# Kernel optimization log

Hardware: AMD Instinct MI355X
Metric: run time of the kernel (lower is better)

The kernel has to match this reference:

```python
import jax, jax.numpy as jnp
import numpy as np

T, B, I, H = 1024, 128, 512, 512
KEEP_PROB = 0.7  # dropout = 0.3


def setup_inputs() -> dict:
    key = jax.random.key(0)
    ks = jax.random.split(key, 8)
    xs = jax.random.normal(ks[0], (T, B, I), dtype=jnp.float32)
    s_in = 1.0 / np.sqrt(I)
    s_h = 1.0 / np.sqrt(H)
    W_ih1 = jax.random.normal(ks[1], (4 * H, I), dtype=jnp.float32) * s_in
    W_hh1 = jax.random.normal(ks[2], (4 * H, H), dtype=jnp.float32) * s_h
    W_ih2 = jax.random.normal(ks[3], (4 * H, H), dtype=jnp.float32) * s_h
    W_hh2 = jax.random.normal(ks[4], (4 * H, H), dtype=jnp.float32) * s_h
    b_ih1 = jnp.zeros((4 * H,), jnp.float32)
    b_hh1 = jnp.zeros((4 * H,), jnp.float32)
    b_ih2 = jnp.zeros((4 * H,), jnp.float32)
    b_hh2 = jnp.zeros((4 * H,), jnp.float32)
    # recurrent dropout mask: same Bernoulli(keep_prob) 0/1 mask for the whole sequence
    mask = jax.random.bernoulli(ks[5], KEEP_PROB, (B, H)).astype(jnp.float32)
    return {"xs": xs, "W_ih1": W_ih1, "W_hh1": W_hh1, "b_ih1": b_ih1, "b_hh1": b_hh1,
            "W_ih2": W_ih2, "W_hh2": W_hh2, "b_ih2": b_ih2, "b_hh2": b_hh2, "mask": mask}


def _lstm_cell(x, h, c, W_ih, W_hh, b_ih, b_hh):
    # PyTorch nn.LSTMCell: gates ordered (i, f, g, o)
    gates = x @ W_ih.T + b_ih + h @ W_hh.T + b_hh  # [B, 4H]
    i, f, g, o = jnp.split(gates, 4, axis=-1)
    c_new = jax.nn.sigmoid(f) * c + jax.nn.sigmoid(i) * jnp.tanh(g)
    h_new = jax.nn.sigmoid(o) * jnp.tanh(c_new)
    return h_new, c_new


def reference(xs, W_ih1, W_hh1, b_ih1, b_hh1, W_ih2, W_hh2, b_ih2, b_hh2, mask):
    drop = mask * (1.0 / KEEP_PROB)  # [B, H]; applied to both h and c (training mode)

    def step(carry, x):
        h1, c1, h2, c2 = carry
        h1, c1 = _lstm_cell(x, h1, c1, W_ih1, W_hh1, b_ih1, b_hh1)
        h1, c1 = h1 * drop, c1 * drop
        h2, c2 = _lstm_cell(h1, h2, c2, W_ih2, W_hh2, b_ih2, b_hh2)
        h2, c2 = h2 * drop, c2 * drop
        return (h1, c1, h2, c2), h2

    z = jnp.zeros((xs.shape[1], W_hh1.shape[1]), xs.dtype)
    init = (z, z, z, z)
    _, hs = jax.lax.scan(step, init, xs)
    return hs  # [T, B, H]
```

## Files before the change

kernel.cpp:

```cpp
#include <hip/hip_runtime.h>
#include <stdint.h>
#include <stddef.h>

typedef unsigned short ushort_t;
typedef __attribute__((ext_vector_type(8))) short short8;
typedef __attribute__((ext_vector_type(4))) float floatx4;

#define T_STEPS 1024
#define BATCH   128
#define HID     512
#define NBLK    128
#define NTHR    512
#define INV_KEEP 1.4285714285714286f

__device__ unsigned g_sync[4096];

struct Params {
  const float* xs;
  const float* Wih1; const float* Whh1; const float* bih1; const float* bhh1;
  const float* Wih2; const float* Whh2; const float* bih2; const float* bhh2;
  const float* mask;
  float* out;
  char* ws;
};

__device__ __forceinline__ void waitgen(unsigned target) {
  if (threadIdx.x < 64) {
    const int l = threadIdx.x;
    for (;;) {
      unsigned a = __hip_atomic_load(&g_sync[l * 32], __ATOMIC_RELAXED,
                                     __HIP_MEMORY_SCOPE_AGENT);
      unsigned b = __hip_atomic_load(&g_sync[(l + 64) * 32], __ATOMIC_RELAXED,
                                     __HIP_MEMORY_SCOPE_AGENT);
      if (__all(a >= target && b >= target)) break;
      __builtin_amdgcn_s_sleep(1);
    }
    __threadfence();
  }
  __syncthreads();
}

__device__ __forceinline__ void postgen(unsigned value) {
  __syncthreads();
  if (threadIdx.x == 0) {
    __threadfence();
    __hip_atomic_store(&g_sync[blockIdx.x * 32], value, __ATOMIC_RELAXED,
                       __HIP_MEMORY_SCOPE_AGENT);
  }
}

__device__ __forceinline__ ushort_t f2b(float a) {
  unsigned u = __float_as_uint(a);
  u += 0x7FFFu + ((u >> 16) & 1u);
  return (ushort_t)(u >> 16);
}

__global__ __launch_bounds__(NTHR, 1) void lstm_persist(Params p) {
  extern __shared__ ushort_t Wl[];

  char* ws = p.ws;
  auto H1HI = [&](int par) { return (ushort_t*)(ws + 524288 + par * 262144); };
  auto H1LO = [&](int par) { return (ushort_t*)(ws + 524288 + par * 262144 + 131072); };
  auto H2HI = [&](int par) { return (ushort_t*)(ws + 1048576 + par * 262144); };
  auto H2LO = [&](int par) { return (ushort_t*)(ws + 1048576 + par * 262144 + 131072); };
  auto XSHI = [&](int par) { return (ushort_t*)(ws + 1572864 + par * 262144); };
  auto XSLO = [&](int par) { return (ushort_t*)(ws + 1572864 + par * 262144 + 131072); };

  const int bid = blockIdx.x, tid = threadIdx.x;
  const int gtid = bid * NTHR + tid;
  const int layer = bid >> 6;
  const int c8 = bid & 63;
  const int lane = tid & 63, w = tid >> 6;
  const int jj = lane & 15, quad = lane >> 4;
  const int rbase = w * 16;

  const float* Wih = layer ? p.Wih2 : p.Wih1;
  const float* Whh = layer ? p.Whh2 : p.Whh1;
  const float* bih = layer ? p.bih2 : p.bih1;
  const float* bhh = layer ? p.bhh2 : p.bhh1;

  for (int i = tid; i < 32768; i += NTHR) {
    int e = i & 7, jjw = (i >> 3) & 15, ntw = (i >> 7) & 1, kg = i >> 8;
    int k = kg * 8 + e;
    int col = ((jjw >> 2) << 9) + c8 * 8 + ntw * 4 + (jjw & 3);
    float wv = (k < 512) ? Wih[col * 512 + k] : Whh[col * 512 + (k - 512)];
    unsigned uw = __float_as_uint(wv);
    Wl[i] = (ushort_t)(uw >> 16);
    float wf = __uint_as_float(uw & 0xFFFF0000u);
    Wl[32768 + i] = f2b(wv - wf);
  }
  {
    uint4 zz = {0u, 0u, 0u, 0u};
    uint4* dst = (uint4*)(ws + 524288);
    for (int i = gtid; i < 65536; i += NBLK * NTHR) dst[i] = zz;
  }
  {
    float v = p.xs[gtid];
    unsigned uv = __float_as_uint(v);
    XSHI(0)[gtid] = (ushort_t)(uv >> 16);
    float hf = __uint_as_float(uv & 0xFFFF0000u);
    XSLO(0)[gtid] = f2b(v - hf);
  }
  float bsum[2];
#pragma unroll
  for (int nt = 0; nt < 2; ++nt) {
    int colW = ((jj >> 2) << 9) + c8 * 8 + nt * 4 + (jj & 3);
    bsum[nt] = bih[colW] + bhh[colW];
  }
  float dpre[2][4];
  float creg[2][4];
#pragma unroll
  for (int nt = 0; nt < 2; ++nt)
#pragma unroll
    for (int e = 0; e < 4; ++e) {
      int r = rbase + quad * 4 + e;
      int hgc = c8 * 8 + nt * 4 + (lane & 3);
      dpre[nt][e] = p.mask[r * 512 + hgc] * INV_KEEP;
      creg[nt][e] = 0.f;
    }

  postgen(1);

  const int rowbyte = ((rbase + jj) * 512 + quad * 8) * 2;
  const bool dostore = (jj < 4);

#pragma unroll 1
  for (unsigned u = 0; u <= T_STEPS; ++u) {
    const bool havex = (u + 2 <= T_STEPS);
    float xv = 0.f;
    if (havex) xv = p.xs[(size_t)(u + 1) * 65536 + gtid];

    waitgen(u + 1);

    if (havex) {
      unsigned uv = __float_as_uint(xv);
      int pn = (u + 1) & 1;
      XSHI(pn)[gtid] = (ushort_t)(uv >> 16);
      float hf = __uint_as_float(uv & 0xFFFF0000u);
      XSLO(pn)[gtid] = f2b(xv - hf);
    }

    const bool active = layer ? (u >= 1) : (u < T_STEPS);
    if (active) {
      const int t = layer ? (int)u - 1 : (int)u;
      const int pu = (int)u & 1, pv = pu ^ 1;
      const ushort_t *aLoHi, *aLoLo, *aHiHi, *aHiLo;
      ushort_t *whHi, *whLo;
      if (layer == 0) {
        aLoHi = XSHI(pu); aLoLo = XSLO(pu);
        aHiHi = H1HI(pv); aHiLo = H1LO(pv);
        whHi = H1HI(pu);  whLo = H1LO(pu);
      } else {
        aLoHi = H1HI(pv); aLoLo = H1LO(pv);
        aHiHi = H2HI(pu); aHiLo = H2LO(pu);
        whHi = H2HI(pv);  whLo = H2LO(pv);
      }

      floatx4 acc[2];
      acc[0] = (floatx4){bsum[0], bsum[0], bsum[0], bsum[0]};
      acc[1] = (floatx4){bsum[1], bsum[1], bsum[1], bsum[1]};

      auto ldchunk = [&](int c, uint4* dst) {
        const char* bh = (const char*)((c < 8) ? aLoHi : aHiHi);
        const char* bl = (const char*)((c < 8) ? aLoLo : aHiLo);
        int kb = (c & 7) * 128;
#pragma unroll
        for (int ks = 0; ks < 2; ++ks) {
          int off = rowbyte + kb + ks * 64;
          dst[ks * 2 + 0] = *(const uint4*)(bh + off);
          dst[ks * 2 + 1] = *(const uint4*)(bl + off);
        }
      };

      uint4 ring[4][4];
      ldchunk(0, ring[0]);
      ldchunk(1, ring[1]);
      ldchunk(2, ring[2]);
#pragma unroll
      for (int c = 0; c < 16; ++c) {
        if (c < 13) ldchunk(c + 3, ring[(c + 3) & 3]);
        uint4* cur = ring[c & 3];
#pragma unroll
        for (int ks = 0; ks < 2; ++ks) {
          short8 ahf = *(const short8*)&cur[ks * 2 + 0];
          short8 alf = *(const short8*)&cur[ks * 2 + 1];
#pragma unroll
          for (int nt = 0; nt < 2; ++nt) {
            int o = (((c * 8 + ks * 4 + quad) * 2 + nt) * 16 + jj) * 8;
            short8 bhf = *(const short8*)&Wl[o];
            short8 blf = *(const short8*)&Wl[32768 + o];
            acc[nt] = __builtin_amdgcn_mfma_f32_16x16x32_bf16(ahf, bhf, acc[nt], 0, 0, 0);
            acc[nt] = __builtin_amdgcn_mfma_f32_16x16x32_bf16(ahf, blf, acc[nt], 0, 0, 0);
            acc[nt] = __builtin_amdgcn_mfma_f32_16x16x32_bf16(alf, bhf, acc[nt], 0, 0, 0);
          }
        }
      }

      const int sb = (lane & 48) | (lane & 3);
#pragma unroll
      for (int nt = 0; nt < 2; ++nt)
#pragma unroll
        for (int e = 0; e < 4; ++e) {
          float v = acc[nt][e];
          float gi = __shfl(v, sb + 0, 64);
          float gf = __shfl(v, sb + 4, 64);
          float gg = __shfl(v, sb + 8, 64);
          float go = __shfl(v, sb + 12, 64);
          float si = 1.f / (1.f + __expf(-gi));
          float sf = 1.f / (1.f + __expf(-gf));
          float so = 1.f / (1.f + __expf(-go));
          float tg = 2.f / (1.f + __expf(-2.f * gg)) - 1.f;
          int r = rbase + quad * 4 + e;
          int hgc = c8 * 8 + nt * 4 + (lane & 3);
          int ci = r * 512 + hgc;
          float cn = sf * creg[nt][e] + si * tg;
          float tc = 2.f / (1.f + __expf(-2.f * cn)) - 1.f;
          float hn = so * tc;
          float d = dpre[nt][e];
          hn *= d; cn *= d;
          creg[nt][e] = cn;
          if (dostore) {
            unsigned uh = __float_as_uint(hn);
            whHi[ci] = (ushort_t)(uh >> 16);
            float hf = __uint_as_float(uh & 0xFFFF0000u);
            whLo[ci] = f2b(hn - hf);
            if (layer) p.out[(size_t)t * 65536 + ci] = hn;
          }
        }
    }
    if (u < T_STEPS) postgen(u + 2);
  }
}

extern "C" void kernel_launch(void* const* d_in, const int* in_sizes, int n_in,
                              void* d_out, int out_size, void* d_ws, size_t ws_size,
                              hipStream_t stream) {
  (void)in_sizes; (void)n_in; (void)out_size; (void)ws_size;
  Params p;
  p.xs   = (const float*)d_in[0];
  p.Wih1 = (const float*)d_in[1];
  p.Whh1 = (const float*)d_in[2];
  p.bih1 = (const float*)d_in[3];
  p.bhh1 = (const float*)d_in[4];
  p.Wih2 = (const float*)d_in[5];
  p.Whh2 = (const float*)d_in[6];
  p.bih2 = (const float*)d_in[7];
  p.bhh2 = (const float*)d_in[8];
  p.mask = (const float*)d_in[9];
  p.out  = (float*)d_out;
  p.ws   = (char*)d_ws;

  static bool attr_done = false;
  if (!attr_done) {
    (void)hipFuncSetAttribute(reinterpret_cast<const void*>(lstm_persist),
                              hipFuncAttributeMaxDynamicSharedMemorySize, 131072);
    attr_done = true;
  }

  void* sym = nullptr;
  hipGetSymbolAddress(&sym, HIP_SYMBOL(g_sync));
  hipMemsetAsync(sym, 0, 4096 * sizeof(unsigned), stream);

  void* args[] = { &p };
  hipLaunchCooperativeKernel(reinterpret_cast<void*>(lstm_persist),
                             dim3(NBLK), dim3(NTHR), args, 131072, stream);
}
```

Measured before the change: 28.52 ms.

## Double block count and split K across warps with LDS reduction

Grid grows from 128 to 256 blocks, so each block covers half the batch rows. The 8 warps split the K dimension in two halves (input part and recurrent part), and the partial sums are combined through an LDS reduction buffer before the gate math. All 8 chunk loads are issued up front with inline-asm global loads and staggered vmcnt waits. The goal is more CUs working per timestep and shorter per-step latency, at the cost of an extra __syncthreads, more LDS, and twice as many blocks in the grid barrier.

```diff
diff --git a/kernel.cpp b/kernel.cpp
--- a/kernel.cpp
+++ b/kernel.cpp
@@ -5,15 +5,16 @@
 typedef unsigned short ushort_t;
 typedef __attribute__((ext_vector_type(8))) short short8;
 typedef __attribute__((ext_vector_type(4))) float floatx4;
+typedef __attribute__((ext_vector_type(4))) unsigned uintx4;
 
 #define T_STEPS 1024
 #define BATCH   128
 #define HID     512
-#define NBLK    128
+#define NBLK    256
 #define NTHR    512
 #define INV_KEEP 1.4285714285714286f
 
-__device__ unsigned g_sync[4096];
+__device__ unsigned g_sync[8192];
 
 struct Params {
   const float* xs;
@@ -32,7 +33,11 @@
                                      __HIP_MEMORY_SCOPE_AGENT);
       unsigned b = __hip_atomic_load(&g_sync[(l + 64) * 32], __ATOMIC_RELAXED,
                                      __HIP_MEMORY_SCOPE_AGENT);
-      if (__all(a >= target && b >= target)) break;
+      unsigned c = __hip_atomic_load(&g_sync[(l + 128) * 32], __ATOMIC_RELAXED,
+                                     __HIP_MEMORY_SCOPE_AGENT);
+      unsigned d = __hip_atomic_load(&g_sync[(l + 192) * 32], __ATOMIC_RELAXED,
+                                     __HIP_MEMORY_SCOPE_AGENT);
+      if (__all(a >= target && b >= target && c >= target && d >= target)) break;
       __builtin_amdgcn_s_sleep(1);
     }
     __threadfence();
@@ -55,7 +60,7 @@
   return (ushort_t)(u >> 16);
 }
 
-__global__ __launch_bounds__(NTHR, 1) void lstm_persist(Params p) {
+__global__ __launch_bounds__(NTHR, 2) void lstm_persist(Params p) {
   extern __shared__ ushort_t Wl[];
 
   char* ws = p.ws;
@@ -68,11 +73,13 @@
 
   const int bid = blockIdx.x, tid = threadIdx.x;
   const int gtid = bid * NTHR + tid;
-  const int layer = bid >> 6;
-  const int c8 = bid & 63;
+  const int layer = bid >> 7;
+  const int c8 = (bid & 127) >> 1;
+  const int bhalf = bid & 1;
   const int lane = tid & 63, w = tid >> 6;
+  const int kh = w >> 2, rg = w & 3;
   const int jj = lane & 15, quad = lane >> 4;
-  const int rbase = w * 16;
+  const int rbase = bhalf * 64 + rg * 16;
 
   const float* Wih = layer ? p.Wih2 : p.Wih1;
   const float* Whh = layer ? p.Whh2 : p.Whh1;
@@ -94,7 +101,7 @@
     uint4* dst = (uint4*)(ws + 524288);
     for (int i = gtid; i < 65536; i += NBLK * NTHR) dst[i] = zz;
   }
-  {
+  if (gtid < 65536) {
     float v = p.xs[gtid];
     unsigned uv = __float_as_uint(v);
     XSHI(0)[gtid] = (ushort_t)(uv >> 16);
@@ -122,11 +129,11 @@
   postgen(1);
 
   const int rowbyte = ((rbase + jj) * 512 + quad * 8) * 2;
-  const bool dostore = (jj < 4);
+  float* red = (float*)((char*)Wl + 131072);
 
 #pragma unroll 1
   for (unsigned u = 0; u <= T_STEPS; ++u) {
-    const bool havex = (u + 2 <= T_STEPS);
+    const bool havex = (u + 2 <= T_STEPS) && (gtid < 65536);
     float xv = 0.f;
     if (havex) xv = p.xs[(size_t)(u + 1) * 65536 + gtid];
 
@@ -155,38 +162,46 @@
         aHiHi = H2HI(pu); aHiLo = H2LO(pu);
         whHi = H2HI(pv);  whLo = H2LO(pv);
       }
+      const char* bh = (const char*)(kh ? aHiHi : aLoHi);
+      const char* bl = (const char*)(kh ? aHiLo : aLoLo);
 
       floatx4 acc[2];
-      acc[0] = (floatx4){bsum[0], bsum[0], bsum[0], bsum[0]};
-      acc[1] = (floatx4){bsum[1], bsum[1], bsum[1], bsum[1]};
-
-      auto ldchunk = [&](int c, uint4* dst) {
-        const char* bh = (const char*)((c < 8) ? aLoHi : aHiHi);
-        const char* bl = (const char*)((c < 8) ? aLoLo : aHiLo);
-        int kb = (c & 7) * 128;
+      if (kh) { acc[0] = (floatx4){0.f, 0.f, 0.f, 0.f}; acc[1] = acc[0]; }
+      else {
+        acc[0] = (floatx4){bsum[0], bsum[0], bsum[0], bsum[0]};
+        acc[1] = (floatx4){bsum[1], bsum[1], bsum[1], bsum[1]};
+      }
+
+      asm volatile("s_waitcnt vmcnt(0)" ::: "memory");
+
+      uintx4 rq[8][4];
+#define ISSUE(C)                                                               \
+  {                                                                            \
+    const char* a0 = bh + rowbyte + (C)*128;                                   \
+    const char* a1 = bl + rowbyte + (C)*128;                                   \
+    asm volatile("global_load_dwordx4 %0, %1, off"                             \
+                 : "=v"(rq[C][0]) : "v"(a0));                                  \
+    asm volatile("global_load_dwordx4 %0, %1, off"                             \
+                 : "=v"(rq[C][1]) : "v"(a1));                                  \
+    asm volatile("global_load_dwordx4 %0, %1, off offset:64"                   \
+                 : "=v"(rq[C][2]) : "v"(a0));                                  \
+    asm volatile("global_load_dwordx4 %0, %1, off offset:64"                   \
+                 : "=v"(rq[C][3]) : "v"(a1));                                  \
+  }
+      ISSUE(0) ISSUE(1) ISSUE(2) ISSUE(3) ISSUE(4) ISSUE(5) ISSUE(6) ISSUE(7)
+#undef ISSUE
+
+      auto dochunk = [&](const uintx4& h0, const uintx4& l0,
+                         const uintx4& h1, const uintx4& l1, int gc) {
 #pragma unroll
         for (int ks = 0; ks < 2; ++ks) {
-          int off = rowbyte + kb + ks * 64;
-          dst[ks * 2 + 0] = *(const uint4*)(bh + off);
-          dst[ks * 2 + 1] = *(const uint4*)(bl + off);
-        }
-      };
-
-      uint4 ring[4][4];
-      ldchunk(0, ring[0]);
-      ldchunk(1, ring[1]);
-      ldchunk(2, ring[2]);
-#pragma unroll
-      for (int c = 0; c < 16; ++c) {
-        if (c < 13) ldchunk(c + 3, ring[(c + 3) & 3]);
-        uint4* cur = ring[c & 3];
-#pragma unroll
-        for (int ks = 0; ks < 2; ++ks) {
-          short8 ahf = *(const short8*)&cur[ks * 2 + 0];
-          short8 alf = *(const short8*)&cur[ks * 2 + 1];
+          const uintx4& ch = ks ? h1 : h0;
+          const uintx4& cl = ks ? l1 : l0;
+          short8 ahf = *(const short8*)&ch;
+          short8 alf = *(const short8*)&cl;
 #pragma unroll
           for (int nt = 0; nt < 2; ++nt) {
-            int o = (((c * 8 + ks * 4 + quad) * 2 + nt) * 16 + jj) * 8;
+            int o = (((gc * 8 + ks * 4 + quad) * 2 + nt) * 16 + jj) * 8;
             short8 bhf = *(const short8*)&Wl[o];
             short8 blf = *(const short8*)&Wl[32768 + o];
             acc[nt] = __builtin_amdgcn_mfma_f32_16x16x32_bf16(ahf, bhf, acc[nt], 0, 0, 0);
@@ -194,39 +209,64 @@
             acc[nt] = __builtin_amdgcn_mfma_f32_16x16x32_bf16(alf, bhf, acc[nt], 0, 0, 0);
           }
         }
+      };
+
+#define CONS(C, NW)                                                            \
+  asm volatile("s_waitcnt vmcnt(" #NW ")");                                    \
+  __builtin_amdgcn_sched_barrier(0);                                           \
+  dochunk(rq[C][0], rq[C][1], rq[C][2], rq[C][3], kh * 8 + (C));
+      CONS(0, 28) CONS(1, 24) CONS(2, 20) CONS(3, 16)
+      CONS(4, 12) CONS(5, 8)  CONS(6, 4)  CONS(7, 0)
+#undef CONS
+
+      if (kh) {
+        int base = (tid - 256) * 9;
+#pragma unroll
+        for (int nt = 0; nt < 2; ++nt)
+#pragma unroll
+          for (int e = 0; e < 4; ++e) red[base + nt * 4 + e] = acc[nt][e];
       }
-
-      const int sb = (lane & 48) | (lane & 3);
-#pragma unroll
-      for (int nt = 0; nt < 2; ++nt)
-#pragma unroll
-        for (int e = 0; e < 4; ++e) {
-          float v = acc[nt][e];
-          float gi = __shfl(v, sb + 0, 64);
-          float gf = __shfl(v, sb + 4, 64);
-          float gg = __shfl(v, sb + 8, 64);
-          float go = __shfl(v, sb + 12, 64);
-          float si = 1.f / (1.f + __expf(-gi));
-          float sf = 1.f / (1.f + __expf(-gf));
-          float so = 1.f / (1.f + __expf(-go));
-          float tg = 2.f / (1.f + __expf(-2.f * gg)) - 1.f;
-          int r = rbase + quad * 4 + e;
-          int hgc = c8 * 8 + nt * 4 + (lane & 3);
-          int ci = r * 512 + hgc;
-          float cn = sf * creg[nt][e] + si * tg;
-          float tc = 2.f / (1.f + __expf(-2.f * cn)) - 1.f;
-          float hn = so * tc;
-          float d = dpre[nt][e];
-          hn *= d; cn *= d;
-          creg[nt][e] = cn;
-          if (dostore) {
-            unsigned uh = __float_as_uint(hn);
-            whHi[ci] = (ushort_t)(uh >> 16);
-            float hf = __uint_as_float(uh & 0xFFFF0000u);
-            whLo[ci] = f2b(hn - hf);
-            if (layer) p.out[(size_t)t * 65536 + ci] = hn;
+      __syncthreads();
+      if (!kh) {
+        int base = tid * 9;
+#pragma unroll
+        for (int nt = 0; nt < 2; ++nt)
+#pragma unroll
+          for (int e = 0; e < 4; ++e) acc[nt][e] += red[base + nt * 4 + e];
+
+        const int sb = (lane & 48) | (lane & 3);
+        const bool dostore = (jj < 4);
+#pragma unroll
+        for (int nt = 0; nt < 2; ++nt)
+#pragma unroll
+          for (int e = 0; e < 4; ++e) {
+            float v = acc[nt][e];
+            float gi = __shfl(v, sb + 0, 64);
+            float gf = __shfl(v, sb + 4, 64);
+            float gg = __shfl(v, sb + 8, 64);
+            float go = __shfl(v, sb + 12, 64);
+            float si = 1.f / (1.f + __expf(-gi));
+            float sf = 1.f / (1.f + __expf(-gf));
+            float so = 1.f / (1.f + __expf(-go));
+            float tg = 2.f / (1.f + __expf(-2.f * gg)) - 1.f;
+            int r = rbase + quad * 4 + e;
+            int hgc = c8 * 8 + nt * 4 + (lane & 3);
+            int ci = r * 512 + hgc;
+            float cn = sf * creg[nt][e] + si * tg;
+            float tc = 2.f / (1.f + __expf(-2.f * cn)) - 1.f;
+            float hn = so * tc;
+            float d = dpre[nt][e];
+            hn *= d; cn *= d;
+            creg[nt][e] = cn;
+            if (dostore) {
+              unsigned uh = __float_as_uint(hn);
+              whHi[ci] = (ushort_t)(uh >> 16);
+              float hf = __uint_as_float(uh & 0xFFFF0000u);
+              whLo[ci] = f2b(hn - hf);
+              if (layer) p.out[(size_t)t * 65536 + ci] = hn;
+            }
           }
-        }
+      }
     }
     if (u < T_STEPS) postgen(u + 2);
   }
@@ -253,15 +293,15 @@
   static bool attr_done = false;
   if (!attr_done) {
     (void)hipFuncSetAttribute(reinterpret_cast<const void*>(lstm_persist),
-                              hipFuncAttributeMaxDynamicSharedMemorySize, 131072);
+                              hipFuncAttributeMaxDynamicSharedMemorySize, 140288);
     attr_done = true;
   }
 
   void* sym = nullptr;
   hipGetSymbolAddress(&sym, HIP_SYMBOL(g_sync));
-  hipMemsetAsync(sym, 0, 4096 * sizeof(unsigned), stream);
+  hipMemsetAsync(sym, 0, 8192 * sizeof(unsigned), stream);
 
   void* args[] = { &p };
   hipLaunchCooperativeKernel(reinterpret_cast<void*>(lstm_persist),
-                             dim3(NBLK), dim3(NTHR), args, 131072, stream);
-}
+                             dim3(NBLK), dim3(NTHR), args, 140288, stream);
+}
```

Result: faster. 24.30 ms (-14.8%).
